# Kernel optimization log

Hardware: AMD Instinct MI355X
Metric: run time of the kernel (lower is better)

## Reference

```python
import jax, jax.numpy as jnp
import numpy as np
import math

B, S, D, H = 2, 2048, 1024, 16
HD = D // H  # head dim = 64


def setup_inputs() -> dict:
    key = jax.random.key(0)
    ks = jax.random.split(key, 8)
    scale = 1.0 / math.sqrt(D)
    return {
        "x": jax.random.normal(ks[0], (B, S, D), dtype=jnp.float32),
        "mask": jax.random.randint(ks[1], (B, S, S), 0, 2).astype(bool),
        "Wq": jax.random.normal(ks[2], (D, D), dtype=jnp.float32) * scale,
        "bq": jax.random.normal(ks[3], (D,), dtype=jnp.float32) * 0.01,
        "Wk": jax.random.normal(ks[4], (D, D), dtype=jnp.float32) * scale,
        "bk": jax.random.normal(ks[5], (D,), dtype=jnp.float32) * 0.01,
        "Wv": jax.random.normal(ks[6], (D, D), dtype=jnp.float32) * scale,
        "bv": jax.random.normal(ks[7], (D,), dtype=jnp.float32) * 0.01,
    }


def reference(x, mask, Wq, bq, Wk, bk, Wv, bv):
    # Linear projections (weights stored as [in, out])
    q = x @ Wq + bq  # [B,S,D]
    k = x @ Wk + bk
    v = x @ Wv + bv
    # split heads -> [B,H,S,HD]
    q = q.reshape(B, S, H, HD).transpose(0, 2, 1, 3)
    k = k.reshape(B, S, H, HD).transpose(0, 2, 1, 3)
    v = v.reshape(B, S, H, HD).transpose(0, 2, 1, 3)
    scores = jnp.einsum("bhqd,bhkd->bhqk", q, k) / jnp.sqrt(jnp.float32(HD))
    # Faithful to the source: masked_fill_(mask, -inf) is immediately
    # overwritten by masked_fill_(mask, 0), so masked positions end up 0
    # BEFORE the softmax (a quirk of the original module).
    scores = jnp.where(mask[:, None, :, :], 0.0, scores)
    attn = jax.nn.softmax(scores, axis=-1)  # dropout=0.0 (eval)
    out = jnp.einsum("bhqk,bhkd->bhqd", attn, v)
    return out.transpose(0, 2, 1, 3).reshape(B, S, D)
```

## Files before the change

### kernel.cpp

```cpp
#include <hip/hip_runtime.h>
#include <cstdint>
#include <cstddef>

static constexpr int B_ = 2, S_ = 2048, D_ = 1024, H_ = 16, HD_ = 64;

typedef float f32x4 __attribute__((ext_vector_type(4)));
typedef short bf16x8 __attribute__((ext_vector_type(8)));

__device__ __forceinline__ unsigned short f2bf(float f) {
    union { float f; unsigned int u; } v; v.f = f;
    unsigned int r = v.u + 0x7FFFu + ((v.u >> 16) & 1u);
    return (unsigned short)(r >> 16);
}

__device__ __forceinline__ unsigned pack2bf(float a, float b) {
#if __has_builtin(__builtin_amdgcn_cvt_pk_bf16_f32)
    auto p = __builtin_amdgcn_cvt_pk_bf16_f32(a, b);
    unsigned u; __builtin_memcpy(&u, &p, 4);
    return u;
#else
    return (unsigned)f2bf(a) | ((unsigned)f2bf(b) << 16);
#endif
}

__device__ __forceinline__ void gload_lds16(const void* g, void* l) {
    __builtin_amdgcn_global_load_lds(
        (const __attribute__((address_space(1))) void*)g,
        (__attribute__((address_space(3))) void*)l, 16, 0, 0);
}

__global__ __launch_bounds__(256)
void cast_x(const float* __restrict__ x, unsigned short* __restrict__ o) {
    size_t i = ((size_t)blockIdx.x * 256 + threadIdx.x) * 8;
    float4 a = *(const float4*)(x + i);
    float4 c = *(const float4*)(x + i + 4);
    uint4 r;
    r.x = pack2bf(a.x, a.y);
    r.y = pack2bf(a.z, a.w);
    r.z = pack2bf(c.x, c.y);
    r.w = pack2bf(c.z, c.w);
    *(uint4*)(o + i) = r;
}

__global__ __launch_bounds__(256)
void mask_pack(const int* __restrict__ m, unsigned char* __restrict__ o) {
    size_t i = ((size_t)blockIdx.x * 256 + threadIdx.x) * 16;
    uint4 r;
    unsigned w[4];
    #pragma unroll
    for (int g = 0; g < 4; ++g) {
        int4 v = *(const int4*)(m + i + g * 4);
        w[g] = (v.x ? 1u : 0u) | (v.y ? 1u << 8 : 0u) |
               (v.z ? 1u << 16 : 0u) | (v.w ? 1u << 24 : 0u);
    }
    r.x = w[0]; r.y = w[1]; r.z = w[2]; r.w = w[3];
    *(uint4*)(o + i) = r;
}

__global__ __launch_bounds__(256)
void transpose_w(const float* __restrict__ Wq, const float* __restrict__ Wk,
                 const float* __restrict__ Wv, unsigned short* __restrict__ wt) {
    const int mat = blockIdx.z;
    const float* __restrict__ W = (mat == 0) ? Wq : (mat == 1) ? Wk : Wv;
    unsigned short* __restrict__ o = wt + (size_t)mat * D_ * D_;
    const int n0 = blockIdx.x * 64, k0 = blockIdx.y * 64;
    __shared__ unsigned short Ts[64][72];
    const int t = threadIdx.x;
    {
        const int nl = t & 63, kb = t >> 6;
        #pragma unroll
        for (int i = 0; i < 16; ++i) {
            int k = kb + i * 4;
            Ts[nl][k] = f2bf(W[(size_t)(k0 + k) * D_ + n0 + nl]);
        }
    }
    __syncthreads();
    {
        const int kl = t & 63, nb = t >> 6;
        #pragma unroll
        for (int i = 0; i < 16; ++i) {
            int n = nb + i * 4;
            o[(size_t)(n0 + n) * D_ + k0 + kl] = Ts[n][kl];
        }
    }
}

__global__ __launch_bounds__(256)
void qkv_gemm(const unsigned short* __restrict__ xb, const unsigned short* __restrict__ wt,
              const float* __restrict__ bq, const float* __restrict__ bk,
              const float* __restrict__ bv,
              unsigned short* __restrict__ qo, unsigned short* __restrict__ ko,
              unsigned short* __restrict__ vto) {
    const int bx = blockIdx.x;
    const int by = blockIdx.y;
    const int mat = bx >> 3;
    const int ncol0 = (bx & 7) * 128;
    const float* __restrict__ bias = (mat == 0) ? bq : (mat == 1) ? bk : bv;
    const unsigned short* __restrict__ Wm = wt + (size_t)mat * D_ * D_;

    __shared__ unsigned short As[128 * 32];
    __shared__ unsigned short Bs[128 * 32];

    const int t = threadIdx.x;
    const int w = t >> 6, lane = t & 63;
    const int l15 = lane & 15, quad = lane >> 4;
    const int mw = (w >> 1) * 64, nw = (w & 1) * 64;
    const int rowBase = by * 128;

    const int srow = lane >> 2;
    const int scol = (lane & 3) * 8;

    f32x4 acc[4][4] = {};

    for (int kt = 0; kt < D_; kt += 32) {
        __syncthreads();
        #pragma unroll
        for (int i = 0; i < 2; ++i) {
            const int r0 = w * 32 + i * 16;
            gload_lds16(xb + (size_t)(rowBase + r0 + srow) * D_ + kt + scol,
                        &As[r0 * 32]);
            gload_lds16(Wm + (size_t)(ncol0 + r0 + srow) * D_ + kt + scol,
                        &Bs[r0 * 32]);
        }
        __syncthreads();

        bf16x8 a[4], b[4];
        #pragma unroll
        for (int i = 0; i < 4; ++i)
            a[i] = *(const bf16x8*)&As[(mw + i * 16 + l15) * 32 + quad * 8];
        #pragma unroll
        for (int j = 0; j < 4; ++j)
            b[j] = *(const bf16x8*)&Bs[(nw + j * 16 + l15) * 32 + quad * 8];
        #pragma unroll
        for (int i = 0; i < 4; ++i)
            #pragma unroll
            for (int j = 0; j < 4; ++j)
                acc[i][j] = __builtin_amdgcn_mfma_f32_16x16x32_bf16(a[i], b[j], acc[i][j], 0, 0, 0);
    }

    if (mat < 2) {
        unsigned short* __restrict__ O = (mat == 0) ? qo : ko;
        const float osc = (mat == 0) ? 0.18033688011112443f : 1.0f;
        #pragma unroll
        for (int j = 0; j < 4; ++j) {
            const int col = ncol0 + nw + j * 16 + l15;
            const float bb = bias[col];
            #pragma unroll
            for (int i = 0; i < 4; ++i)
                #pragma unroll
                for (int r = 0; r < 4; ++r) {
                    const int m = rowBase + mw + i * 16 + quad * 4 + r;
                    O[(size_t)m * D_ + col] = f2bf((acc[i][j][r] + bb) * osc);
                }
        }
    } else {
        #pragma unroll
        for (int j = 0; j < 4; ++j) {
            const int col = ncol0 + nw + j * 16 + l15;
            const float bb = bias[col];
            const int hh = col >> 6, hd = col & 63;
            #pragma unroll
            for (int i = 0; i < 4; ++i) {
                const int m0 = rowBase + mw + i * 16 + quad * 4;
                const int bg = m0 >> 11, s0 = m0 & 2047;
                ushort4 pk;
                pk.x = f2bf(acc[i][j][0] + bb);
                pk.y = f2bf(acc[i][j][1] + bb);
                pk.z = f2bf(acc[i][j][2] + bb);
                pk.w = f2bf(acc[i][j][3] + bb);
                *(ushort4*)&vto[(((size_t)bg * H_ + hh) * HD_ + hd) * S_ + s0] = pk;
            }
        }
    }
}

__global__ __launch_bounds__(256, 4)
void attn_mfma(const unsigned short* __restrict__ qmat,
               const unsigned short* __restrict__ kmat,
               const unsigned short* __restrict__ vtg,
               const unsigned char* __restrict__ msk, float* __restrict__ out) {
    const int h = blockIdx.x, qt = blockIdx.y, b = blockIdx.z;
    const int t = threadIdx.x, w = t >> 6, lane = t & 63;
    const int l15 = lane & 15, quad = lane >> 4;
    const int q0 = qt * 128;

    __shared__ __align__(16) unsigned short Ks[64][72];
    __shared__ __align__(16) unsigned short Vt[64][72];
    __shared__ __align__(16) unsigned short Ps[128][72];

    const size_t bh = (size_t)b * S_ * D_ + (size_t)h * HD_;
    const unsigned short* __restrict__ qp = qmat + bh;
    const unsigned short* __restrict__ kp = kmat + bh;
    const unsigned short* __restrict__ vp = vtg + ((size_t)b * H_ + h) * HD_ * S_;
    const unsigned char* __restrict__ mb = msk + (size_t)b * S_ * S_;

    bf16x8 qfr[2][2];
    #pragma unroll
    for (int nt = 0; nt < 2; ++nt)
        #pragma unroll
        for (int kst = 0; kst < 2; ++kst)
            qfr[nt][kst] = *(const bf16x8*)(qp +
                (size_t)(q0 + w * 32 + nt * 16 + l15) * D_ + kst * 32 + quad * 8);

    f32x4 accO[2][4] = {};
    f32x4 lsA[2] = {};
    bf16x8 ones;
    #pragma unroll
    for (int i = 0; i < 8; ++i) ones[i] = (short)0x3F80;

    const int rstage = t >> 2, cstage = (t & 3) * 16;

    for (int kt = 0; kt < S_; kt += 64) {
        __syncthreads();
        *(uint4*)&Ks[rstage][cstage]     = *(const uint4*)(kp + (size_t)(kt + rstage) * D_ + cstage);
        *(uint4*)&Ks[rstage][cstage + 8] = *(const uint4*)(kp + (size_t)(kt + rstage) * D_ + cstage + 8);
        *(uint4*)&Vt[rstage][cstage]     = *(const uint4*)(vp + (size_t)rstage * S_ + kt + cstage);
        *(uint4*)&Vt[rstage][cstage + 8] = *(const uint4*)(vp + (size_t)rstage * S_ + kt + cstage + 8);
        __syncthreads();

        f32x4 sc[4][2] = {};
        #pragma unroll
        for (int kst = 0; kst < 2; ++kst) {
            bf16x8 kfr[4];
            #pragma unroll
            for (int mt = 0; mt < 4; ++mt)
                kfr[mt] = *(const bf16x8*)&Ks[mt * 16 + l15][kst * 32 + quad * 8];
            #pragma unroll
            for (int mt = 0; mt < 4; ++mt)
                #pragma unroll
                for (int nt = 0; nt < 2; ++nt)
                    sc[mt][nt] = __builtin_amdgcn_mfma_f32_16x16x32_bf16(kfr[mt], qfr[nt][kst], sc[mt][nt], 0, 0, 0);
        }

        #pragma unroll
        for (int nt = 0; nt < 2; ++nt) {
            const int qr = w * 32 + nt * 16 + l15;
            const unsigned char* __restrict__ mrow = mb + (size_t)(q0 + qr) * S_ + kt;
            #pragma unroll
            for (int mt = 0; mt < 4; ++mt) {
                const unsigned mu = *(const unsigned*)(mrow + mt * 16 + quad * 4);
                float p[4];
                #pragma unroll
                for (int r = 0; r < 4; ++r) {
                    float e = __builtin_amdgcn_exp2f(sc[mt][nt][r]);
                    p[r] = ((mu >> (8 * r)) & 0xFFu) ? 1.0f : e;
                }
                uint2 pk;
                pk.x = pack2bf(p[0], p[1]);
                pk.y = pack2bf(p[2], p[3]);
                *(uint2*)&Ps[qr][mt * 16 + quad * 4] = pk;
            }
        }

        #pragma unroll
        for (int kst = 0; kst < 2; ++kst) {
            bf16x8 vfr[4];
            #pragma unroll
            for (int dt = 0; dt < 4; ++dt)
                vfr[dt] = *(const bf16x8*)&Vt[dt * 16 + l15][kst * 32 + quad * 8];
            #pragma unroll
            for (int mt = 0; mt < 2; ++mt) {
                bf16x8 pfr = *(const bf16x8*)&Ps[w * 32 + mt * 16 + l15][kst * 32 + quad * 8];
                #pragma unroll
                for (int dt = 0; dt < 4; ++dt)
                    accO[mt][dt] = __builtin_amdgcn_mfma_f32_16x16x32_bf16(pfr, vfr[dt], accO[mt][dt], 0, 0, 0);
                lsA[mt] = __builtin_amdgcn_mfma_f32_16x16x32_bf16(pfr, ones, lsA[mt], 0, 0, 0);
            }
        }
    }

    float* __restrict__ ob = out + ((size_t)b * S_ + q0) * D_ + (size_t)h * HD_;
    #pragma unroll
    for (int mt = 0; mt < 2; ++mt)
        #pragma unroll
        for (int r = 0; r < 4; ++r) {
            const float inv = 1.0f / lsA[mt][r];
            const int qr = w * 32 + mt * 16 + quad * 4 + r;
            #pragma unroll
            for (int dt = 0; dt < 4; ++dt)
                ob[(size_t)qr * D_ + dt * 16 + l15] = accO[mt][dt][r] * inv;
        }
}

extern "C" void kernel_launch(void* const* d_in, const int* in_sizes, int n_in,
                              void* d_out, int out_size, void* d_ws, size_t ws_size,
                              hipStream_t stream) {
    (void)in_sizes; (void)n_in; (void)out_size; (void)ws_size;
    const float* x    = (const float*)d_in[0];
    const int*   mask = (const int*)d_in[1];
    const float* Wq   = (const float*)d_in[2];
    const float* bq   = (const float*)d_in[3];
    const float* Wk   = (const float*)d_in[4];
    const float* bk   = (const float*)d_in[5];
    const float* Wv   = (const float*)d_in[6];
    const float* bv   = (const float*)d_in[7];
    float* out = (float*)d_out;

    const size_t M1 = (size_t)1024 * 1024;
    unsigned short* xb  = (unsigned short*)d_ws;
    unsigned short* wtb = xb + 4 * M1;
    unsigned short* qb  = wtb + 3 * M1;
    unsigned short* kb  = qb + 4 * M1;
    unsigned short* vtb = kb + 4 * M1;
    unsigned char*  mk  = (unsigned char*)(vtb + 4 * M1);

    cast_x<<<2048, 256, 0, stream>>>(x, xb);
    mask_pack<<<2048, 256, 0, stream>>>(mask, mk);
    transpose_w<<<dim3(16, 16, 3), 256, 0, stream>>>(Wq, Wk, Wv, wtb);
    qkv_gemm<<<dim3(24, 32), 256, 0, stream>>>(xb, wtb, bq, bk, bv, qb, kb, vtb);
    attn_mfma<<<dim3(16, 16, 2), 256, 0, stream>>>(qb, kb, vtb, mk, out);
}
```

Baseline: 252.5 us.

## Double-buffer GEMM and attention tiles with swizzled LDS and merged prep kernel

```diff
diff --git a/kernel.cpp b/kernel.cpp
--- a/kernel.cpp
+++ b/kernel.cpp
@@ -30,57 +30,54 @@
 }
 
 __global__ __launch_bounds__(256)
-void cast_x(const float* __restrict__ x, unsigned short* __restrict__ o) {
-    size_t i = ((size_t)blockIdx.x * 256 + threadIdx.x) * 8;
-    float4 a = *(const float4*)(x + i);
-    float4 c = *(const float4*)(x + i + 4);
-    uint4 r;
-    r.x = pack2bf(a.x, a.y);
-    r.y = pack2bf(a.z, a.w);
-    r.z = pack2bf(c.x, c.y);
-    r.w = pack2bf(c.z, c.w);
-    *(uint4*)(o + i) = r;
-}
-
-__global__ __launch_bounds__(256)
-void mask_pack(const int* __restrict__ m, unsigned char* __restrict__ o) {
-    size_t i = ((size_t)blockIdx.x * 256 + threadIdx.x) * 16;
-    uint4 r;
-    unsigned w[4];
-    #pragma unroll
-    for (int g = 0; g < 4; ++g) {
-        int4 v = *(const int4*)(m + i + g * 4);
-        w[g] = (v.x ? 1u : 0u) | (v.y ? 1u << 8 : 0u) |
-               (v.z ? 1u << 16 : 0u) | (v.w ? 1u << 24 : 0u);
-    }
-    r.x = w[0]; r.y = w[1]; r.z = w[2]; r.w = w[3];
-    *(uint4*)(o + i) = r;
-}
-
-__global__ __launch_bounds__(256)
-void transpose_w(const float* __restrict__ Wq, const float* __restrict__ Wk,
-                 const float* __restrict__ Wv, unsigned short* __restrict__ wt) {
-    const int mat = blockIdx.z;
-    const float* __restrict__ W = (mat == 0) ? Wq : (mat == 1) ? Wk : Wv;
-    unsigned short* __restrict__ o = wt + (size_t)mat * D_ * D_;
-    const int n0 = blockIdx.x * 64, k0 = blockIdx.y * 64;
+void prep(const float* __restrict__ x, unsigned short* __restrict__ xo,
+          const int* __restrict__ m, unsigned char* __restrict__ mo,
+          const float* __restrict__ Wq, const float* __restrict__ Wk,
+          const float* __restrict__ Wv, unsigned short* __restrict__ wt) {
     __shared__ unsigned short Ts[64][72];
-    const int t = threadIdx.x;
-    {
-        const int nl = t & 63, kb = t >> 6;
-        #pragma unroll
-        for (int i = 0; i < 16; ++i) {
-            int k = kb + i * 4;
-            Ts[nl][k] = f2bf(W[(size_t)(k0 + k) * D_ + n0 + nl]);
-        }
-    }
-    __syncthreads();
-    {
-        const int kl = t & 63, nb = t >> 6;
-        #pragma unroll
-        for (int i = 0; i < 16; ++i) {
-            int n = nb + i * 4;
-            o[(size_t)(n0 + n) * D_ + k0 + kl] = Ts[n][kl];
+    const int bid = blockIdx.x, t = threadIdx.x;
+    if (bid < 2048) {
+        size_t i = ((size_t)bid * 256 + t) * 8;
+        float4 a = *(const float4*)(x + i);
+        float4 c = *(const float4*)(x + i + 4);
+        uint4 r;
+        r.x = pack2bf(a.x, a.y); r.y = pack2bf(a.z, a.w);
+        r.z = pack2bf(c.x, c.y); r.w = pack2bf(c.z, c.w);
+        *(uint4*)(xo + i) = r;
+    } else if (bid < 4096) {
+        size_t i = ((size_t)(bid - 2048) * 256 + t) * 16;
+        uint4 r;
+        unsigned w[4];
+        #pragma unroll
+        for (int g = 0; g < 4; ++g) {
+            int4 v = *(const int4*)(m + i + g * 4);
+            w[g] = (v.x ? 1u : 0u) | (v.y ? 1u << 8 : 0u) |
+                   (v.z ? 1u << 16 : 0u) | (v.w ? 1u << 24 : 0u);
+        }
+        r.x = w[0]; r.y = w[1]; r.z = w[2]; r.w = w[3];
+        *(uint4*)(mo + i) = r;
+    } else {
+        const int tid = bid - 4096;
+        const int mat = tid >> 8, tile = tid & 255;
+        const float* __restrict__ W = (mat == 0) ? Wq : (mat == 1) ? Wk : Wv;
+        unsigned short* __restrict__ o = wt + (size_t)mat * D_ * D_;
+        const int n0 = (tile & 15) * 64, k0 = (tile >> 4) * 64;
+        {
+            const int nl = t & 63, kb = t >> 6;
+            #pragma unroll
+            for (int i = 0; i < 16; ++i) {
+                int k = kb + i * 4;
+                Ts[nl][k] = f2bf(W[(size_t)(k0 + k) * D_ + n0 + nl]);
+            }
+        }
+        __syncthreads();
+        {
+            const int kl = t & 63, nb = t >> 6;
+            #pragma unroll
+            for (int i = 0; i < 16; ++i) {
+                int n = nb + i * 4;
+                o[(size_t)(n0 + n) * D_ + k0 + kl] = Ts[n][kl];
+            }
         }
     }
 }
@@ -98,8 +95,8 @@
     const float* __restrict__ bias = (mat == 0) ? bq : (mat == 1) ? bk : bv;
     const unsigned short* __restrict__ Wm = wt + (size_t)mat * D_ * D_;
 
-    __shared__ unsigned short As[128 * 32];
-    __shared__ unsigned short Bs[128 * 32];
+    __shared__ unsigned short As[2][128 * 32];
+    __shared__ unsigned short Bs[2][128 * 32];
 
     const int t = threadIdx.x;
     const int w = t >> 6, lane = t & 63;
@@ -107,30 +104,42 @@
     const int mw = (w >> 1) * 64, nw = (w & 1) * 64;
     const int rowBase = by * 128;
 
-    const int srow = lane >> 2;
-    const int scol = (lane & 3) * 8;
+    const int r16 = lane >> 2;
+    const int sslot = lane & 3;
+    const int sg = (sslot ^ ((r16 >> 1) & 3)) * 8;
+    const int rcol = (quad ^ ((l15 >> 1) & 3)) * 8;
 
     f32x4 acc[4][4] = {};
 
-    for (int kt = 0; kt < D_; kt += 32) {
+    #pragma unroll
+    for (int j = 0; j < 2; ++j) {
+        const int r0 = w * 32 + j * 16;
+        gload_lds16(xb + (size_t)(rowBase + r0 + r16) * D_ + sg, &As[0][r0 * 32]);
+        gload_lds16(Wm + (size_t)(ncol0 + r0 + r16) * D_ + sg, &Bs[0][r0 * 32]);
+    }
+
+    for (int it = 0; it < 32; ++it) {
+        const int cur = it & 1;
         __syncthreads();
-        #pragma unroll
-        for (int i = 0; i < 2; ++i) {
-            const int r0 = w * 32 + i * 16;
-            gload_lds16(xb + (size_t)(rowBase + r0 + srow) * D_ + kt + scol,
-                        &As[r0 * 32]);
-            gload_lds16(Wm + (size_t)(ncol0 + r0 + srow) * D_ + kt + scol,
-                        &Bs[r0 * 32]);
-        }
-        __syncthreads();
+        if (it + 1 < 32) {
+            const int ktn = (it + 1) * 32;
+            #pragma unroll
+            for (int j = 0; j < 2; ++j) {
+                const int r0 = w * 32 + j * 16;
+                gload_lds16(xb + (size_t)(rowBase + r0 + r16) * D_ + ktn + sg,
+                            &As[cur ^ 1][r0 * 32]);
+                gload_lds16(Wm + (size_t)(ncol0 + r0 + r16) * D_ + ktn + sg,
+                            &Bs[cur ^ 1][r0 * 32]);
+            }
+        }
 
         bf16x8 a[4], b[4];
         #pragma unroll
         for (int i = 0; i < 4; ++i)
-            a[i] = *(const bf16x8*)&As[(mw + i * 16 + l15) * 32 + quad * 8];
+            a[i] = *(const bf16x8*)&As[cur][(mw + i * 16 + l15) * 32 + rcol];
         #pragma unroll
         for (int j = 0; j < 4; ++j)
-            b[j] = *(const bf16x8*)&Bs[(nw + j * 16 + l15) * 32 + quad * 8];
+            b[j] = *(const bf16x8*)&Bs[cur][(nw + j * 16 + l15) * 32 + rcol];
         #pragma unroll
         for (int i = 0; i < 4; ++i)
             #pragma unroll
@@ -174,7 +183,7 @@
     }
 }
 
-__global__ __launch_bounds__(256, 4)
+__global__ __launch_bounds__(256)
 void attn_mfma(const unsigned short* __restrict__ qmat,
                const unsigned short* __restrict__ kmat,
                const unsigned short* __restrict__ vtg,
@@ -184,8 +193,8 @@
     const int l15 = lane & 15, quad = lane >> 4;
     const int q0 = qt * 128;
 
-    __shared__ __align__(16) unsigned short Ks[64][72];
-    __shared__ __align__(16) unsigned short Vt[64][72];
+    __shared__ unsigned short Ks[2][64 * 64];
+    __shared__ unsigned short Vs[2][64 * 64];
     __shared__ __align__(16) unsigned short Ps[128][72];
 
     const size_t bh = (size_t)b * S_ * D_ + (size_t)h * HD_;
@@ -194,6 +203,9 @@
     const unsigned short* __restrict__ vp = vtg + ((size_t)b * H_ + h) * HD_ * S_;
     const unsigned char* __restrict__ mb = msk + (size_t)b * S_ * S_;
 
+    const int rs = lane >> 3, sslot = lane & 7;
+    const int sg = (sslot ^ rs) * 8;
+
     bf16x8 qfr[2][2];
     #pragma unroll
     for (int nt = 0; nt < 2; ++nt)
@@ -208,23 +220,47 @@
     #pragma unroll
     for (int i = 0; i < 8; ++i) ones[i] = (short)0x3F80;
 
-    const int rstage = t >> 2, cstage = (t & 3) * 16;
-
-    for (int kt = 0; kt < S_; kt += 64) {
+    #pragma unroll
+    for (int j = 0; j < 2; ++j) {
+        const int rb = w * 16 + j * 8;
+        gload_lds16(kp + (size_t)(rb + rs) * D_ + sg, &Ks[0][rb * 64]);
+        gload_lds16(vp + (size_t)(rb + rs) * S_ + sg, &Vs[0][rb * 64]);
+    }
+
+    for (int it = 0; it < 32; ++it) {
+        const int cur = it & 1;
+        const int kt = it * 64;
         __syncthreads();
-        *(uint4*)&Ks[rstage][cstage]     = *(const uint4*)(kp + (size_t)(kt + rstage) * D_ + cstage);
-        *(uint4*)&Ks[rstage][cstage + 8] = *(const uint4*)(kp + (size_t)(kt + rstage) * D_ + cstage + 8);
-        *(uint4*)&Vt[rstage][cstage]     = *(const uint4*)(vp + (size_t)rstage * S_ + kt + cstage);
-        *(uint4*)&Vt[rstage][cstage + 8] = *(const uint4*)(vp + (size_t)rstage * S_ + kt + cstage + 8);
-        __syncthreads();
+
+        unsigned mu[2][4];
+        #pragma unroll
+        for (int nt = 0; nt < 2; ++nt) {
+            const int qr = w * 32 + nt * 16 + l15;
+            const unsigned char* __restrict__ mrow = mb + (size_t)(q0 + qr) * S_ + kt;
+            #pragma unroll
+            for (int mt = 0; mt < 4; ++mt)
+                mu[nt][mt] = *(const unsigned*)(mrow + mt * 16 + quad * 4);
+        }
+
+        if (it + 1 < 32) {
+            const int ktn = kt + 64;
+            #pragma unroll
+            for (int j = 0; j < 2; ++j) {
+                const int rb = w * 16 + j * 8;
+                gload_lds16(kp + (size_t)(ktn + rb + rs) * D_ + sg, &Ks[cur ^ 1][rb * 64]);
+                gload_lds16(vp + (size_t)(rb + rs) * S_ + ktn + sg, &Vs[cur ^ 1][rb * 64]);
+            }
+        }
 
         f32x4 sc[4][2] = {};
         #pragma unroll
         for (int kst = 0; kst < 2; ++kst) {
             bf16x8 kfr[4];
             #pragma unroll
-            for (int mt = 0; mt < 4; ++mt)
-                kfr[mt] = *(const bf16x8*)&Ks[mt * 16 + l15][kst * 32 + quad * 8];
+            for (int mt = 0; mt < 4; ++mt) {
+                const int R = mt * 16 + l15;
+                kfr[mt] = *(const bf16x8*)&Ks[cur][R * 64 + (((kst * 4 + quad) ^ (l15 & 7)) * 8)];
+            }
             #pragma unroll
             for (int mt = 0; mt < 4; ++mt)
                 #pragma unroll
@@ -235,15 +271,13 @@
         #pragma unroll
         for (int nt = 0; nt < 2; ++nt) {
             const int qr = w * 32 + nt * 16 + l15;
-            const unsigned char* __restrict__ mrow = mb + (size_t)(q0 + qr) * S_ + kt;
             #pragma unroll
             for (int mt = 0; mt < 4; ++mt) {
-                const unsigned mu = *(const unsigned*)(mrow + mt * 16 + quad * 4);
                 float p[4];
                 #pragma unroll
                 for (int r = 0; r < 4; ++r) {
                     float e = __builtin_amdgcn_exp2f(sc[mt][nt][r]);
-                    p[r] = ((mu >> (8 * r)) & 0xFFu) ? 1.0f : e;
+                    p[r] = ((mu[nt][mt] >> (8 * r)) & 0xFFu) ? 1.0f : e;
                 }
                 uint2 pk;
                 pk.x = pack2bf(p[0], p[1]);
@@ -256,8 +290,10 @@
         for (int kst = 0; kst < 2; ++kst) {
             bf16x8 vfr[4];
             #pragma unroll
-            for (int dt = 0; dt < 4; ++dt)
-                vfr[dt] = *(const bf16x8*)&Vt[dt * 16 + l15][kst * 32 + quad * 8];
+            for (int dt = 0; dt < 4; ++dt) {
+                const int R = dt * 16 + l15;
+                vfr[dt] = *(const bf16x8*)&Vs[cur][R * 64 + (((kst * 4 + quad) ^ (l15 & 7)) * 8)];
+            }
             #pragma unroll
             for (int mt = 0; mt < 2; ++mt) {
                 bf16x8 pfr = *(const bf16x8*)&Ps[w * 32 + mt * 16 + l15][kst * 32 + quad * 8];
@@ -304,9 +340,7 @@
     unsigned short* vtb = kb + 4 * M1;
     unsigned char*  mk  = (unsigned char*)(vtb + 4 * M1);
 
-    cast_x<<<2048, 256, 0, stream>>>(x, xb);
-    mask_pack<<<2048, 256, 0, stream>>>(mask, mk);
-    transpose_w<<<dim3(16, 16, 3), 256, 0, stream>>>(Wq, Wk, Wv, wtb);
+    prep<<<4864, 256, 0, stream>>>(x, xb, mask, mk, Wq, Wk, Wv, wtb);
     qkv_gemm<<<dim3(24, 32), 256, 0, stream>>>(xb, wtb, bq, bk, bv, qb, kb, vtb);
     attn_mfma<<<dim3(16, 16, 2), 256, 0, stream>>>(qb, kb, vtb, mk, out);
 }
```

Result: faster. 234.7 us (-7.1%).
